# Kernel optimization log

Hardware: AMD Instinct MI355X
Metric: run time of the kernel (lower is better)

## Reference

```python
import jax, jax.numpy as jnp
import numpy as np

N_NODES = 100000
N_GRAPHS = 64

def gcn_conv(x, edge_index, W, b, num_nodes):
    # PyG GCNConv: x' = D^-1/2 (A + I) D^-1/2 (x W) + b
    h = x @ W  # [N, out]
    row, col = edge_index[0], edge_index[1]
    loops = jnp.arange(num_nodes, dtype=row.dtype)
    src = jnp.concatenate([row, loops])  # message source (x_j)
    dst = jnp.concatenate([col, loops])  # aggregation target
    deg = jax.ops.segment_sum(jnp.ones_like(src, dtype=h.dtype), dst,
                              num_segments=num_nodes)
    dinv = jnp.where(deg > 0, jax.lax.rsqrt(deg), 0.0)
    norm = dinv[src] * dinv[dst]  # [E+N]
    msgs = h[src] * norm[:, None]  # gather-transform
    out = jax.ops.segment_sum(msgs, dst, num_segments=num_nodes)  # scatter
    return out + b

def global_mean_pool(x, batch, num_graphs):
    sums = jax.ops.segment_sum(x, batch, num_segments=num_graphs)
    cnts = jax.ops.segment_sum(jnp.ones((x.shape[0],), x.dtype), batch,
                               num_segments=num_graphs)
    return sums / jnp.maximum(cnts, 1.0)[:, None]

def setup_inputs() -> dict:
    key = jax.random.key(0)
    ks = jax.random.split(key, 12)
    d_in, d_hid, d_mid, d_out = 128, 128, 20, 10
    n_edges = 1600000
    x = jax.random.normal(ks[0], (N_NODES, d_in), dtype=jnp.float32)
    edge_index = jax.random.randint(ks[1], (2, n_edges), 0, N_NODES, dtype=jnp.int64)
    batch = jnp.sort(jax.random.randint(ks[2], (N_NODES,), 0, N_GRAPHS, dtype=jnp.int64))
    def glorot(k, fan_in, fan_out):
        s = (6.0 / (fan_in + fan_out)) ** 0.5
        return jax.random.uniform(k, (fan_in, fan_out), jnp.float32, -s, s)
    return {
        "x": x, "edge_index": edge_index, "batch": batch,
        "W1": glorot(ks[3], d_in, d_hid), "b1": jnp.zeros((d_hid,), jnp.float32),
        "W2": glorot(ks[4], d_hid, d_hid), "b2": jnp.zeros((d_hid,), jnp.float32),
        "fc1_W": glorot(ks[5], d_hid, d_mid), "fc1_b": jnp.zeros((d_mid,), jnp.float32),
        "fc2_W": glorot(ks[6], d_mid, d_out), "fc2_b": jnp.zeros((d_out,), jnp.float32),
    }

def reference(x, edge_index, batch, W1, b1, W2, b2, fc1_W, fc1_b, fc2_W, fc2_b):
    # eval mode: dropout is identity
    h = gcn_conv(x, edge_index, W1, b1, N_NODES)
    h = jax.nn.elu(h)
    h = gcn_conv(h, edge_index, W2, b2, N_NODES)
    g = global_mean_pool(h, batch, N_GRAPHS)  # [G, hidden]
    g = jax.nn.relu(g @ fc1_W + fc1_b)
    g = g @ fc2_W + fc2_b
    return jax.nn.log_softmax(g, axis=1)
```

## Files before the change

kernel.cpp:

```cpp
#include <hip/hip_runtime.h>
#include <math.h>

#define DH 128
#define BCAP 16384

typedef __bf16 bf8_t __attribute__((ext_vector_type(8)));
typedef short short8 __attribute__((ext_vector_type(8)));
typedef float f4_t __attribute__((ext_vector_type(4)));
typedef float f2_t __attribute__((ext_vector_type(2)));

__device__ inline unsigned short f2b(float f) {
    unsigned int u = __builtin_bit_cast(unsigned int, f);
    u = u + 0x7fffu + ((u >> 16) & 1u);
    return (unsigned short)(u >> 16);
}
__device__ inline float b2f(unsigned short h) {
    return __builtin_bit_cast(float, (unsigned int)h << 16);
}

__global__ __launch_bounds__(256) void k_bucket(const int* __restrict__ row,
                                                const int* __restrict__ col,
                                                int E, int nbuck, int chunk,
                                                unsigned int* __restrict__ pairs,
                                                int* __restrict__ bcur) {
    __shared__ int lcnt[256];
    __shared__ int lbase[256];
    __shared__ unsigned int srec[8192];
    int t = threadIdx.x;
    int e0 = blockIdx.x * chunk;
    int e1 = min(e0 + chunk, E);
    lcnt[t] = 0;
    __syncthreads();
    for (int i = e0 + t; i < e1; i += 256) {
        int d = col[i];
        int b = d >> 9;
        int slot = atomicAdd(&lcnt[b], 1);
        srec[i - e0] = ((unsigned int)b << 22) | ((unsigned int)(d & 511) << 13)
                     | (unsigned int)slot;
    }
    __syncthreads();
    if (t < nbuck) {
        int c = lcnt[t];
        lbase[t] = (c > 0) ? atomicAdd(&bcur[t * 16], c) : 0;
    }
    __syncthreads();
    for (int i = e0 + t; i < e1; i += 256) {
        unsigned int r = srec[i - e0];
        int b = r >> 22;
        unsigned int dl = (r >> 13) & 511u;
        int slot = (int)(r & 8191u);
        int g = lbase[b] + slot;
        if (g < BCAP)
            pairs[(size_t)b * BCAP + g] = ((unsigned int)row[i] << 9) | dl;
    }
}

__global__ __launch_bounds__(256) void k_build(const unsigned int* __restrict__ pairs,
                                               const int* __restrict__ bcur,
                                               int nbuck, int N,
                                               int* __restrict__ off,
                                               float* __restrict__ dinv,
                                               int* __restrict__ csr) {
    __shared__ int sb[256];
    __shared__ int cnt2[512];
    __shared__ int excl[512];
    __shared__ int curi[512];
    __shared__ int stmp[256];
    int b = blockIdx.x, t = threadIdx.x;
    sb[t] = (t < nbuck) ? min(bcur[t * 16], BCAP) : 0;
    __syncthreads();
    for (int d = 1; d < 256; d <<= 1) {
        int v = (t >= d) ? sb[t - d] : 0;
        __syncthreads();
        sb[t] += v;
        __syncthreads();
    }
    int base = (b == 0) ? 0 : sb[b - 1];
    int cnt = sb[b] - base;
    int node0 = b << 9;
    int nodes = min(512, N - node0);
    cnt2[t] = 0; cnt2[t + 256] = 0;
    __syncthreads();
    const unsigned int* pp = pairs + (size_t)b * BCAP;
    for (int i = t; i < cnt; i += 256)
        atomicAdd(&cnt2[pp[i] & 511u], 1);
    __syncthreads();
    stmp[t] = cnt2[2 * t] + cnt2[2 * t + 1];
    __syncthreads();
    for (int d = 1; d < 256; d <<= 1) {
        int v = (t >= d) ? stmp[t - d] : 0;
        __syncthreads();
        stmp[t] += v;
        __syncthreads();
    }
    int pre = (t == 0) ? 0 : stmp[t - 1];
    excl[2 * t] = pre;
    excl[2 * t + 1] = pre + cnt2[2 * t];
    __syncthreads();
    if (t < nodes) {
        off[node0 + t] = base + excl[t];
        dinv[node0 + t] = rsqrtf((float)(cnt2[t] + 1));
    }
    int t2 = t + 256;
    if (t2 < nodes) {
        off[node0 + t2] = base + excl[t2];
        dinv[node0 + t2] = rsqrtf((float)(cnt2[t2] + 1));
    }
    if (t == 0) off[node0 + nodes] = base + cnt;
    curi[t] = excl[t]; curi[t + 256] = excl[t + 256];
    __syncthreads();
    for (int i = t; i < cnt; i += 256) {
        unsigned int p = pp[i];
        int d = (int)(p & 511u);
        int slot = atomicAdd(&curi[d], 1);
        csr[base + slot] = (int)(p >> 9);
    }
}

__global__ void k_prepW(const float* __restrict__ W1, const float* __restrict__ W2,
                        unsigned short* __restrict__ Wt1, unsigned short* __restrict__ Wt2) {
    int t = blockIdx.x * blockDim.x + threadIdx.x;
    const float* W = (t < 16384) ? W1 : W2;
    unsigned short* Wt = (t < 16384) ? Wt1 : Wt2;
    int v = t & 16383;
    int k = v >> 7, n = v & 127;
    Wt[n * DH + k] = f2b(W[k * DH + n]);
}

__global__ __launch_bounds__(256) void k_gemm_mfma(const void* __restrict__ Xin, int x_is_bf16,
                                                   const unsigned short* __restrict__ Wt,
                                                   const float* __restrict__ dinv,
                                                   unsigned char* __restrict__ Y, int nrows) {
    __shared__ unsigned short Xs[64 * 136];
    __shared__ unsigned short Ws[128 * 136];
    int t = threadIdx.x;
    int row0 = blockIdx.x * 64;

    for (int v = t; v < 128 * 32; v += 256) {
        int n = v >> 5, kq = v & 31;
        ushort4 w = ((const ushort4*)Wt)[v];
        *(ushort4*)&Ws[n * 136 + kq * 4] = w;
    }
    if (x_is_bf16) {
        const unsigned short* X = (const unsigned short*)Xin;
        for (int v = t; v < 64 * 32; v += 256) {
            int r = v >> 5, cq = v & 31;
            int gr = row0 + r;
            ushort4 h;
            if (gr < nrows) h = ((const ushort4*)X)[(size_t)gr * 32 + cq];
            else { h.x = 0; h.y = 0; h.z = 0; h.w = 0; }
            *(ushort4*)&Xs[r * 136 + cq * 4] = h;
        }
    } else {
        const float* X = (const float*)Xin;
        for (int v = t; v < 64 * 32; v += 256) {
            int r = v >> 5, cq = v & 31;
            int gr = row0 + r;
            ushort4 h;
            if (gr < nrows) {
                float4 xv = ((const float4*)X)[(size_t)gr * 32 + cq];
                h.x = f2b(xv.x); h.y = f2b(xv.y); h.z = f2b(xv.z); h.w = f2b(xv.w);
            } else { h.x = 0; h.y = 0; h.z = 0; h.w = 0; }
            *(ushort4*)&Xs[r * 136 + cq * 4] = h;
        }
    }
    __syncthreads();

    int w = t >> 6;
    int lane = t & 63;
    int quad = lane >> 4;
    int l16 = lane & 15;
    int rw = w * 16;

    f4_t acc[8];
#pragma unroll
    for (int j = 0; j < 8; j++) acc[j] = (f4_t){0.f, 0.f, 0.f, 0.f};

#pragma unroll
    for (int kk = 0; kk < 4; kk++) {
        int k0 = kk * 32;
        bf8_t a = __builtin_bit_cast(bf8_t,
            *(const short8*)&Xs[(rw + l16) * 136 + k0 + quad * 8]);
#pragma unroll
        for (int j = 0; j < 8; j++) {
            bf8_t b = __builtin_bit_cast(bf8_t,
                *(const short8*)&Ws[(j * 16 + l16) * 136 + k0 + quad * 8]);
            acc[j] = __builtin_amdgcn_mfma_f32_16x16x32_bf16(a, b, acc[j], 0, 0, 0);
        }
    }

#pragma unroll
    for (int reg = 0; reg < 4; reg++) {
        int r = row0 + rw + quad * 4 + reg;
        if (r < nrows) {
            float dv = dinv[r];
            float v0 = acc[0][reg] * dv, v1 = acc[1][reg] * dv;
            float v2 = acc[2][reg] * dv, v3 = acc[3][reg] * dv;
            float v4 = acc[4][reg] * dv, v5 = acc[5][reg] * dv;
            float v6 = acc[6][reg] * dv, v7 = acc[7][reg] * dv;
            int d0 = __builtin_amdgcn_cvt_pk_fp8_f32(v0, v1, 0, false);
            d0 = __builtin_amdgcn_cvt_pk_fp8_f32(v2, v3, d0, true);
            int d1 = __builtin_amdgcn_cvt_pk_fp8_f32(v4, v5, 0, false);
            d1 = __builtin_amdgcn_cvt_pk_fp8_f32(v6, v7, d1, true);
            *(uint2*)&Y[(size_t)r * DH + l16 * 8] = make_uint2((unsigned)d0, (unsigned)d1);
        }
    }
}

__global__ __launch_bounds__(256) void k_aggm(const unsigned char* __restrict__ T,
                                              unsigned short* __restrict__ Out,
                                              const float* __restrict__ dinv,
                                              const int* __restrict__ off,
                                              const int* __restrict__ csr,
                                              const float* __restrict__ bias,
                                              int elu, int N) {
    __shared__ int ofs[17];
    __shared__ float dinv16[16];
    __shared__ float bias_l[128];
    __shared__ unsigned int lidx[768];
    __shared__ unsigned char ldst[768];
    __shared__ unsigned int Bt4[2][32][34];
    __shared__ unsigned char Al[2][16][48];

    int t = threadIdx.x;
    int d0 = blockIdx.x * 16;
    if (t < 17) ofs[t] = off[min(d0 + t, N)];
    if (t < 16) dinv16[t] = dinv[d0 + t];
    if (t < 128) bias_l[t] = bias[((t & 7) << 4) | (t >> 3)];
    __syncthreads();
    int s0 = ofs[0];
    int cnt = min(ofs[16] - s0, 752);
    for (int k = t; k < cnt; k += 256) {
        lidx[k] = (unsigned)csr[s0 + k];
        int p = s0 + k, d = 0;
#pragma unroll
        for (int i = 1; i < 16; i++) d += (p >= ofs[i]) ? 1 : 0;
        ldst[k] = (unsigned char)d;
    }
    if (t < 16) { lidx[cnt + t] = (unsigned)(d0 + t); ldst[cnt + t] = (unsigned char)t; }
    int ncnt = cnt + 16;
    int pcnt = (ncnt + 31) & ~31;
    for (int k = ncnt + t; k < pcnt; k += 256) { lidx[k] = (unsigned)d0; ldst[k] = 0xFF; }
    __syncthreads();

    int w = t >> 6;
    int lane = t & 63;
    int q = lane >> 4;
    int l16 = lane & 15;
    int el = t >> 3;
    int seg = t & 7;
    int nch = pcnt >> 5;
    int x = l16 & 3;
    unsigned int selp = (unsigned)(x | ((x + 4) << 8));

    auto stage = [&](int c, int bf) {
        if (t < 128) {
            int m = t >> 3;
            int k0 = (t & 7) * 4;
            unsigned int ld = *(const unsigned int*)&ldst[c * 32 + k0];
            unsigned int u = ld ^ (0x01010101u * (unsigned)m);
            unsigned int z = (u - 0x01010101u) & ~u & 0x80808080u;
            *(unsigned int*)&Al[bf][m][k0] = (z >> 7) * 0x38u;
        }
        unsigned int j = lidx[c * 32 + el];
        uint4 r = ((const uint4*)(T + (size_t)j * DH))[seg];
        Bt4[bf][seg * 4 + 0][el] = r.x;
        Bt4[bf][seg * 4 + 1][el] = r.y;
        Bt4[bf][seg * 4 + 2][el] = r.z;
        Bt4[bf][seg * 4 + 3][el] = r.w;
    };

    f4_t acc0 = (f4_t){0.f, 0.f, 0.f, 0.f};
    f4_t acc1 = (f4_t){0.f, 0.f, 0.f, 0.f};

    stage(0, 0);
    __syncthreads();
    for (int c = 0; c < nch; c++) {
        int bf = c & 1;
        long al = __builtin_bit_cast(long, *(const uint2*)&Al[bf][l16][q * 8]);
#pragma unroll
        for (int cb = 0; cb < 2; cb++) {
            int cq = 8 * w + cb * 4 + (l16 >> 2);
            const unsigned int* bp = &Bt4[bf][cq][q * 8];
            uint2 e01 = *(const uint2*)bp;
            uint2 e23 = *(const uint2*)(bp + 2);
            uint2 e45 = *(const uint2*)(bp + 4);
            uint2 e67 = *(const uint2*)(bp + 6);
            unsigned t01 = __builtin_amdgcn_perm(e01.y, e01.x, selp);
            unsigned t23 = __builtin_amdgcn_perm(e23.y, e23.x, selp);
            unsigned t45 = __builtin_amdgcn_perm(e45.y, e45.x, selp);
            unsigned t67 = __builtin_amdgcn_perm(e67.y, e67.x, selp);
            uint2 bfrag;
            bfrag.x = __builtin_amdgcn_perm(t23, t01, 0x05040100u);
            bfrag.y = __builtin_amdgcn_perm(t67, t45, 0x05040100u);
            long bl = __builtin_bit_cast(long, bfrag);
            if (cb == 0)
                acc0 = __builtin_amdgcn_mfma_f32_16x16x32_fp8_fp8(al, bl, acc0, 0, 0, 0);
            else
                acc1 = __builtin_amdgcn_mfma_f32_16x16x32_fp8_fp8(al, bl, acc1, 0, 0, 0);
        }
        if (c + 1 < nch) stage(c + 1, 1 - bf);
        __syncthreads();
    }

#pragma unroll
    for (int cb = 0; cb < 2; cb++) {
        f4_t acc = cb ? acc1 : acc0;
        int np = 32 * w + cb * 16 + l16;
        int ctrue = ((np & 7) << 4) | (np >> 3);
        float bs = bias_l[np];
#pragma unroll
        for (int reg = 0; reg < 4; reg++) {
            int m = q * 4 + reg;
            int nd = d0 + m;
            if (nd < N) {
                float o = acc[reg] * dinv16[m] + bs;
                if (elu) o = o > 0.f ? o : expm1f(o);
                Out[(size_t)nd * DH + ctrue] = f2b(o);
            }
        }
    }
}

__global__ __launch_bounds__(256) void k_pool(const unsigned int* __restrict__ H32,
                                              const int* __restrict__ batch,
                                              float* __restrict__ Gsum,
                                              int* __restrict__ cnts, int N) {
    int g = blockIdx.x;
    int p = blockIdx.y;
    int t = threadIdx.x;
    int lane = t & 63;
    int rg = t >> 6;
    int lo = 0, hi = N;
    while (lo < hi) { int m = (lo + hi) >> 1; if (batch[m] < g) lo = m + 1; else hi = m; }
    int s = lo;
    hi = N;
    while (lo < hi) { int m = (lo + hi) >> 1; if (batch[m] < g + 1) lo = m + 1; else hi = m; }
    int e = lo;
    int len = e - s;
    int parts = (int)gridDim.y;
    int chunk = (len + parts - 1) / parts;
    int i0 = s + p * chunk;
    int i1 = min(i0 + chunk, e);
    float a0 = 0.f, a1 = 0.f;
    for (int i = i0 + rg; i < i1; i += 4) {
        unsigned int v = H32[(size_t)i * 64 + lane];
        a0 += b2f((unsigned short)(v & 0xffffu));
        a1 += b2f((unsigned short)(v >> 16));
    }
    __shared__ float ps[4][DH];
    ps[rg][lane * 2] = a0;
    ps[rg][lane * 2 + 1] = a1;
    __syncthreads();
    if (t < DH) {
        float v = ps[0][t] + ps[1][t] + ps[2][t] + ps[3][t];
        atomicAdd(&Gsum[g * DH + t], v);
    }
    if (p == 0 && t == 0) cnts[g] = len;
}

__global__ __launch_bounds__(64) void k_head(const float* __restrict__ Gsum,
                                             const int* __restrict__ cnts,
                                             const float* __restrict__ W1,
                                             const float* __restrict__ b1,
                                             const float* __restrict__ W2,
                                             const float* __restrict__ b2,
                                             float* __restrict__ out) {
    int g = blockIdx.x;
    int t = threadIdx.x;
    __shared__ float gv[DH];
    __shared__ float mid[20];
    __shared__ float o[10];
    float inv = 1.f / fmaxf((float)cnts[g], 1.f);
    for (int i = t; i < DH; i += 64) gv[i] = Gsum[g * DH + i] * inv;
    __syncthreads();
    if (t < 20) {
        float a = b1[t];
        for (int k = 0; k < DH; k++) a += gv[k] * W1[k * 20 + t];
        mid[t] = fmaxf(a, 0.f);
    }
    __syncthreads();
    if (t < 10) {
        float a = b2[t];
        for (int k = 0; k < 20; k++) a += mid[k] * W2[k * 10 + t];
        o[t] = a;
    }
    __syncthreads();
    if (t == 0) {
        float m = -1e30f;
        for (int j = 0; j < 10; j++) m = fmaxf(m, o[j]);
        float ssum = 0.f;
        for (int j = 0; j < 10; j++) ssum += expf(o[j] - m);
        float l = logf(ssum);
        for (int j = 0; j < 10; j++) out[g * 10 + j] = o[j] - m - l;
    }
}

extern "C" void kernel_launch(void* const* d_in, const int* in_sizes, int n_in,
                              void* d_out, int out_size, void* d_ws, size_t ws_size,
                              hipStream_t stream) {
    const float* x    = (const float*)d_in[0];
    const int*   ei   = (const int*)d_in[1];
    const int*   batch= (const int*)d_in[2];
    const float* W1   = (const float*)d_in[3];
    const float* b1   = (const float*)d_in[4];
    const float* W2   = (const float*)d_in[5];
    const float* b2   = (const float*)d_in[6];
    const float* fc1W = (const float*)d_in[7];
    const float* fc1b = (const float*)d_in[8];
    const float* fc2W = (const float*)d_in[9];
    const float* fc2b = (const float*)d_in[10];
    float* out = (float*)d_out;

    int N = in_sizes[0] / DH;
    int E = in_sizes[1] / 2;
    int G = out_size / 10;

    char* p = (char*)d_ws;
    auto alloc = [&](size_t bytes) {
        char* r = p;
        p += (bytes + 255) & ~(size_t)255;
        return r;
    };
    unsigned char*  t8 = (unsigned char*)alloc((size_t)N * DH);
    unsigned short* a1 = (unsigned short*)alloc((size_t)N * DH * 2);
    int*   csr  = (int*)alloc((size_t)E * 4);
    int*   off  = (int*)alloc((size_t)(N + 1) * 4);
    float* dinv = (float*)alloc((size_t)N * 4);
    int nbuck = (N + 511) >> 9;
    unsigned int* pairs = (unsigned int*)alloc((size_t)nbuck * BCAP * 4);
    unsigned short* Wt1 = (unsigned short*)alloc(DH * DH * 2);
    unsigned short* Wt2 = (unsigned short*)alloc(DH * DH * 2);
    float* Gsum = (float*)alloc((size_t)G * DH * 4);
    int*   bcur = (int*)alloc(256 * 16 * 4);
    int*   cnts = (int*)alloc((size_t)G * 4);

    const int* row = ei;
    const int* col = ei + E;

    (void)hipMemsetAsync(Gsum, 0, (size_t)G * DH * 4 + 256 * 16 * 4, stream);

    const int chunk = 8192;
    int ablocks = (E + chunk - 1) / chunk;
    k_bucket<<<ablocks, 256, 0, stream>>>(row, col, E, nbuck, chunk, pairs, bcur);
    k_build<<<nbuck, 256, 0, stream>>>(pairs, bcur, nbuck, N, off, dinv, csr);
    k_prepW<<<128, 256, 0, stream>>>(W1, W2, Wt1, Wt2);

    int gblocks = (N + 63) / 64;
    int mblocks = (N + 15) / 16;
    k_gemm_mfma<<<gblocks, 256, 0, stream>>>(x, 0, Wt1, dinv, t8, N);
    k_aggm<<<mblocks, 256, 0, stream>>>(t8, a1, dinv, off, csr, b1, 1, N);
    k_gemm_mfma<<<gblocks, 256, 0, stream>>>(a1, 1, Wt2, dinv, t8, N);
    k_aggm<<<mblocks, 256, 0, stream>>>(t8, a1, dinv, off, csr, b2, 0, N);

    dim3 pg(G, 32);
    k_pool<<<pg, 256, 0, stream>>>((const unsigned int*)a1, batch, Gsum, cnts, N);
    k_head<<<G, 64, 0, stream>>>(Gsum, cnts, fc1W, fc1b, fc2W, fc2b, out);
}
```

Before: 315.8 us.

## Split aggregation chunks across warps, truncate fp32-to-bf16 with perm, halve bucket chunk

The aggregation kernel now hands whole 32-edge chunks to each of the four warps, one per warp. Each warp gathers its chunk into registers, transposes it into its own shared-memory tile and accumulates all 128 output columns in eight MFMA accumulators. This replaces the block-wide barrier after every chunk with a single cross-warp reduction through shared memory at the end. The GEMM's fp32-to-bf16 input conversion switches from round-to-nearest to byte-permute truncation, which slightly changes numerics. The bucketing kernel uses half-size chunks and shared buffers, so it launches twice as many blocks with more occupancy.

```diff
diff --git a/kernel.cpp b/kernel.cpp
--- a/kernel.cpp
+++ b/kernel.cpp
@@ -25,7 +25,7 @@
                                                 int* __restrict__ bcur) {
     __shared__ int lcnt[256];
     __shared__ int lbase[256];
-    __shared__ unsigned int srec[8192];
+    __shared__ unsigned int srec[4096];
     int t = threadIdx.x;
     int e0 = blockIdx.x * chunk;
     int e1 = min(e0 + chunk, E);
@@ -156,12 +156,15 @@
         for (int v = t; v < 64 * 32; v += 256) {
             int r = v >> 5, cq = v & 31;
             int gr = row0 + r;
-            ushort4 h;
+            uint2 hv;
             if (gr < nrows) {
                 float4 xv = ((const float4*)X)[(size_t)gr * 32 + cq];
-                h.x = f2b(xv.x); h.y = f2b(xv.y); h.z = f2b(xv.z); h.w = f2b(xv.w);
-            } else { h.x = 0; h.y = 0; h.z = 0; h.w = 0; }
-            *(ushort4*)&Xs[r * 136 + cq * 4] = h;
+                hv.x = __builtin_amdgcn_perm(__builtin_bit_cast(unsigned, xv.y),
+                                             __builtin_bit_cast(unsigned, xv.x), 0x07060302u);
+                hv.y = __builtin_amdgcn_perm(__builtin_bit_cast(unsigned, xv.w),
+                                             __builtin_bit_cast(unsigned, xv.z), 0x07060302u);
+            } else { hv.x = 0; hv.y = 0; }
+            *(uint2*)&Xs[r * 136 + cq * 4] = hv;
         }
     }
     __syncthreads();
@@ -217,10 +220,10 @@
     __shared__ int ofs[17];
     __shared__ float dinv16[16];
     __shared__ float bias_l[128];
-    __shared__ unsigned int lidx[768];
-    __shared__ unsigned char ldst[768];
-    __shared__ unsigned int Bt4[2][32][34];
-    __shared__ unsigned char Al[2][16][48];
+    __shared__ __align__(16) unsigned char pool_[32768];
+    unsigned int* lidx = (unsigned int*)(pool_ + 20480);
+    unsigned char* ldst = pool_ + 23552;
+    float* Red = (float*)pool_;
 
     int t = threadIdx.x;
     int d0 = blockIdx.x * 16;
@@ -247,41 +250,57 @@
     int lane = t & 63;
     int q = lane >> 4;
     int l16 = lane & 15;
-    int el = t >> 3;
-    int seg = t & 7;
+    int es = lane >> 3;
+    int seg = lane & 7;
     int nch = pcnt >> 5;
+
+    unsigned int* Bt = (unsigned int*)(pool_ + w * 5120);
+    unsigned char* Al = pool_ + w * 5120 + 4352;
+
+    f4_t acc[8];
+#pragma unroll
+    for (int j = 0; j < 8; j++) acc[j] = (f4_t){0.f, 0.f, 0.f, 0.f};
+
+    uint4 R[4];
+    auto gather = [&](int c) {
+#pragma unroll
+        for (int p = 0; p < 4; p++) {
+            unsigned int j = lidx[c * 32 + p * 8 + es];
+            R[p] = ((const uint4*)(T + (size_t)j * DH))[seg];
+        }
+    };
+
     int x = l16 & 3;
     unsigned int selp = (unsigned)(x | ((x + 4) << 8));
 
-    auto stage = [&](int c, int bf) {
-        if (t < 128) {
-            int m = t >> 3;
-            int k0 = (t & 7) * 4;
-            unsigned int ld = *(const unsigned int*)&ldst[c * 32 + k0];
-            unsigned int u = ld ^ (0x01010101u * (unsigned)m);
-            unsigned int z = (u - 0x01010101u) & ~u & 0x80808080u;
-            *(unsigned int*)&Al[bf][m][k0] = (z >> 7) * 0x38u;
-        }
-        unsigned int j = lidx[c * 32 + el];
-        uint4 r = ((const uint4*)(T + (size_t)j * DH))[seg];
-        Bt4[bf][seg * 4 + 0][el] = r.x;
-        Bt4[bf][seg * 4 + 1][el] = r.y;
-        Bt4[bf][seg * 4 + 2][el] = r.z;
-        Bt4[bf][seg * 4 + 3][el] = r.w;
-    };
-
-    f4_t acc0 = (f4_t){0.f, 0.f, 0.f, 0.f};
-    f4_t acc1 = (f4_t){0.f, 0.f, 0.f, 0.f};
-
-    stage(0, 0);
-    __syncthreads();
-    for (int c = 0; c < nch; c++) {
-        int bf = c & 1;
-        long al = __builtin_bit_cast(long, *(const uint2*)&Al[bf][l16][q * 8]);
-#pragma unroll
-        for (int cb = 0; cb < 2; cb++) {
-            int cq = 8 * w + cb * 4 + (l16 >> 2);
-            const unsigned int* bp = &Bt4[bf][cq][q * 8];
+    int c = w;
+    if (c < nch) gather(c);
+    for (; c < nch; c += 4) {
+#pragma unroll
+        for (int p = 0; p < 4; p++) {
+            unsigned int rr[4] = {R[p].x, R[p].y, R[p].z, R[p].w};
+#pragma unroll
+            for (int dq = 0; dq < 4; dq++)
+                Bt[(seg * 4 + dq) * 34 + p * 8 + es] = rr[dq];
+        }
+        {
+            int m = lane >> 2;
+            int k0 = (lane & 3) * 8;
+            uint2 ld = *(const uint2*)&ldst[c * 32 + k0];
+            unsigned um = 0x01010101u * (unsigned)m;
+            unsigned u0 = ld.x ^ um, u1 = ld.y ^ um;
+            unsigned z0 = (u0 - 0x01010101u) & ~u0 & 0x80808080u;
+            unsigned z1 = (u1 - 0x01010101u) & ~u1 & 0x80808080u;
+            uint2 av;
+            av.x = (z0 >> 7) * 0x38u;
+            av.y = (z1 >> 7) * 0x38u;
+            *(uint2*)&Al[m * 48 + k0] = av;
+        }
+        if (c + 4 < nch) gather(c + 4);
+        long al = __builtin_bit_cast(long, *(const uint2*)&Al[l16 * 48 + q * 8]);
+#pragma unroll
+        for (int cb = 0; cb < 8; cb++) {
+            const unsigned int* bp = &Bt[(cb * 4 + (l16 >> 2)) * 34 + q * 8];
             uint2 e01 = *(const uint2*)bp;
             uint2 e23 = *(const uint2*)(bp + 2);
             uint2 e45 = *(const uint2*)(bp + 4);
@@ -294,30 +313,30 @@
             bfrag.x = __builtin_amdgcn_perm(t23, t01, 0x05040100u);
             bfrag.y = __builtin_amdgcn_perm(t67, t45, 0x05040100u);
             long bl = __builtin_bit_cast(long, bfrag);
-            if (cb == 0)
-                acc0 = __builtin_amdgcn_mfma_f32_16x16x32_fp8_fp8(al, bl, acc0, 0, 0, 0);
-            else
-                acc1 = __builtin_amdgcn_mfma_f32_16x16x32_fp8_fp8(al, bl, acc1, 0, 0, 0);
-        }
-        if (c + 1 < nch) stage(c + 1, 1 - bf);
-        __syncthreads();
-    }
-
-#pragma unroll
-    for (int cb = 0; cb < 2; cb++) {
-        f4_t acc = cb ? acc1 : acc0;
-        int np = 32 * w + cb * 16 + l16;
-        int ctrue = ((np & 7) << 4) | (np >> 3);
-        float bs = bias_l[np];
-#pragma unroll
-        for (int reg = 0; reg < 4; reg++) {
-            int m = q * 4 + reg;
-            int nd = d0 + m;
-            if (nd < N) {
-                float o = acc[reg] * dinv16[m] + bs;
-                if (elu) o = o > 0.f ? o : expm1f(o);
-                Out[(size_t)nd * DH + ctrue] = f2b(o);
-            }
+            acc[cb] = __builtin_amdgcn_mfma_f32_16x16x32_fp8_fp8(al, bl, acc[cb], 0, 0, 0);
+        }
+    }
+    __syncthreads();
+
+#pragma unroll
+    for (int cb = 0; cb < 8; cb++)
+#pragma unroll
+        for (int reg = 0; reg < 4; reg++)
+            Red[(w * 16 + q * 4 + reg) * 128 + cb * 16 + l16] = acc[cb][reg];
+    __syncthreads();
+
+#pragma unroll
+    for (int i = 0; i < 8; i++) {
+        int idx = i * 256 + t;
+        int m = idx >> 7, np = idx & 127;
+        float v = Red[(0 * 16 + m) * 128 + np] + Red[(1 * 16 + m) * 128 + np]
+                + Red[(2 * 16 + m) * 128 + np] + Red[(3 * 16 + m) * 128 + np];
+        int nd = d0 + m;
+        if (nd < N) {
+            float o = v * dinv16[m] + bias_l[np];
+            if (elu) o = o > 0.f ? o : expm1f(o);
+            int ctrue = ((np & 7) << 4) | (np >> 3);
+            Out[(size_t)nd * DH + ctrue] = f2b(o);
         }
     }
 }
@@ -440,7 +459,7 @@
 
     (void)hipMemsetAsync(Gsum, 0, (size_t)G * DH * 4 + 256 * 16 * 4, stream);
 
-    const int chunk = 8192;
+    const int chunk = 4096;
     int ablocks = (E + chunk - 1) / chunk;
     k_bucket<<<ablocks, 256, 0, stream>>>(row, col, E, nbuck, chunk, pairs, bcur);
     k_build<<<nbuck, 256, 0, stream>>>(pairs, bcur, nbuck, N, off, dinv, csr);
```

New measurement: 320.9 us. About the same (+1.6%).
